# Performance work log

Measured on AMD Instinct MI355X. Metric: run time of the kernel, lower is better.

Reference implementation:

```python
import jax, jax.numpy as jnp
import numpy as np

ALPHA = 2.0
K_HOPS = 3
N_NODES, N_EDGES, IN_DIM = 8192, 131072, 128


def _mlp(coeffs, W0, W1, W2, W3):
    # MLP(n_layers=n_hidden_layers+2=4, relu between, no bias, bn/dropout off in eval)
    h = jax.nn.relu(coeffs @ W0)
    h = jax.nn.relu(h @ W1)
    h = jax.nn.relu(h @ W2)
    return h @ W3  # [N, 1] rotation angles


def _aggregate_k_hop(edge_index, angles):
    # Faithful translation of aggregate_k_hop including its in-place aliasing:
    # enhanced_angles aliases angles, and step_k ACCUMULATES across hops
    # (torch_scatter reduces into the provided out tensor).
    N = angles.shape[0]
    row, col = edge_index[0], edge_index[1]
    f = lambda k: jnp.exp(jnp.asarray(-ALPHA * k, angles.dtype))
    # hop 1: scatter-add over the raw edge list (duplicate edges counted, as in original)
    step = jax.ops.segment_sum(angles[col] * f(1), row, num_segments=N)
    enhanced = angles + step
    # Dense boolean adjacency: composing paths then np.unique(axis=1) is exactly the
    # 'exists a k-step walk' indicator, i.e. boolean adjacency powers.
    adj = jnp.zeros((N, N), jnp.float32).at[row, col].set(1.0)
    P = adj
    for k in range(2, K_HOPS + 1):
        P = ((P @ adj) > 0).astype(jnp.float32)  # unique k-walk pairs
        step = step + f(k) * (P @ enhanced)      # reads angles AFTER previous in-place add
        enhanced = enhanced + step               # step accumulates across hops
    return enhanced


def setup_inputs() -> dict:
    key = jax.random.key(0)
    k0, k1, k2, k3, k4, k5 = jax.random.split(key, 6)
    s = 1.0 / np.sqrt(IN_DIM)
    return {
        "coeffs": jax.random.normal(k0, (N_NODES, IN_DIM), jnp.float32),
        "W0": jax.random.normal(k1, (IN_DIM, IN_DIM), jnp.float32) * s,
        "W1": jax.random.normal(k2, (IN_DIM, IN_DIM), jnp.float32) * s,
        "W2": jax.random.normal(k3, (IN_DIM, IN_DIM), jnp.float32) * s,
        "W3": jax.random.normal(k4, (IN_DIM, 1), jnp.float32) * s,
        "edge_index": jax.random.randint(k5, (2, N_EDGES), 0, N_NODES, dtype=jnp.int32),
    }


def reference(coeffs, W0, W1, W2, W3, edge_index):
    angles = _mlp(coeffs, W0, W1, W2, W3)
    return _aggregate_k_hop(edge_index, angles)  # batch.node_rotation_angles, [N, 1]
```

## Files before the change

### kernel.cpp

```cpp
#include <hip/hip_runtime.h>

constexpr int N    = 8192;
constexpr int NE   = 131072;
constexpr int WPR  = N / 32;
constexpr int MAXD = 64;

#define F1 0.13533528323661270f
#define F2 0.018315638888734179f
#define F3 0.0024787521766663585f

using bf16x8 = __attribute__((ext_vector_type(8))) short;
using f32x4  = __attribute__((ext_vector_type(4))) float;

__device__ __forceinline__ unsigned short f2bf(float f) {
    unsigned int u = __float_as_uint(f);
    u = (u + 0x7FFFu + ((u >> 16) & 1u)) >> 16;
    return (unsigned short)u;
}

__global__ __launch_bounds__(256) void mlp_kernel(
    const float* __restrict__ X,
    const float* __restrict__ W0, const float* __restrict__ W1,
    const float* __restrict__ W2, const float* __restrict__ W3,
    float* __restrict__ angles, uint4* __restrict__ zbase)
{
    __shared__ unsigned short Xb[32 * 136];
    __shared__ unsigned short Wt[128 * 136];
    __shared__ float part[2][32];

    const int tid  = threadIdx.x;
    const int row0 = blockIdx.x * 32;
    const int w  = tid >> 6, l = tid & 63;
    const int mt = w & 1, nh = w >> 1;
    const int lm = l & 15, lq = l >> 4;

    if (tid < 16) {
        uint4 z; z.x = z.y = z.z = z.w = 0u;
        zbase[blockIdx.x * 16 + tid] = z;
    }

    for (int q = tid; q < 32 * 32; q += 256) {
        float4 v = *(const float4*)&X[row0 * 128 + q * 4];
        ushort4 b;
        b.x = f2bf(v.x); b.y = f2bf(v.y); b.z = f2bf(v.z); b.w = f2bf(v.w);
        *(ushort4*)&Xb[(q >> 5) * 136 + (q & 31) * 4] = b;
    }

    for (int layer = 0; layer < 3; ++layer) {
        const float* __restrict__ W = (layer == 0) ? W0 : (layer == 1) ? W1 : W2;
        for (int it = 0; it < 16; ++it) {
            int flat = it * 256 + tid;
            int n  = flat & 127;
            int k0 = (flat >> 7) << 2;
            ushort4 b;
            b.x = f2bf(W[(k0 + 0) * 128 + n]);
            b.y = f2bf(W[(k0 + 1) * 128 + n]);
            b.z = f2bf(W[(k0 + 2) * 128 + n]);
            b.w = f2bf(W[(k0 + 3) * 128 + n]);
            *(ushort4*)&Wt[n * 136 + k0] = b;
        }
        __syncthreads();

        f32x4 acc[4];
#pragma unroll
        for (int t = 0; t < 4; ++t) acc[t] = (f32x4){0.f, 0.f, 0.f, 0.f};

#pragma unroll
        for (int kc = 0; kc < 4; ++kc) {
            bf16x8 a = *(const bf16x8*)&Xb[(mt * 16 + lm) * 136 + kc * 32 + lq * 8];
#pragma unroll
            for (int t = 0; t < 4; ++t) {
                bf16x8 b = *(const bf16x8*)
                    &Wt[(nh * 64 + t * 16 + lm) * 136 + kc * 32 + lq * 8];
                acc[t] = __builtin_amdgcn_mfma_f32_16x16x32_bf16(a, b, acc[t], 0, 0, 0);
            }
        }

#pragma unroll
        for (int t = 0; t < 4; ++t)
#pragma unroll
            for (int r = 0; r < 4; ++r) acc[t][r] = fmaxf(acc[t][r], 0.0f);

        __syncthreads();

        if (layer < 2) {
#pragma unroll
            for (int t = 0; t < 4; ++t)
#pragma unroll
                for (int r = 0; r < 4; ++r)
                    Xb[(mt * 16 + lq * 4 + r) * 136 + nh * 64 + t * 16 + lm] =
                        f2bf(acc[t][r]);
        } else {
            float p[4] = {0.f, 0.f, 0.f, 0.f};
#pragma unroll
            for (int t = 0; t < 4; ++t) {
                float w3v = W3[nh * 64 + t * 16 + lm];
#pragma unroll
                for (int r = 0; r < 4; ++r) p[r] += acc[t][r] * w3v;
            }
#pragma unroll
            for (int r = 0; r < 4; ++r) {
                p[r] += __shfl_xor(p[r], 1, 64);
                p[r] += __shfl_xor(p[r], 2, 64);
                p[r] += __shfl_xor(p[r], 4, 64);
                p[r] += __shfl_xor(p[r], 8, 64);
            }
            if (lm == 0)
#pragma unroll
                for (int r = 0; r < 4; ++r)
                    part[nh][mt * 16 + lq * 4 + r] = p[r];
            __syncthreads();
            if (tid < 32) angles[row0 + tid] = part[0][tid] + part[1][tid];
        }
    }
}

__global__ void edges_kernel(const int* __restrict__ ei,
                             const float* __restrict__ angles,
                             float* __restrict__ s1,
                             int* __restrict__ cnt_g,
                             int* __restrict__ nbr_g)
{
    int e = blockIdx.x * blockDim.x + threadIdx.x;
    if (e < NE) {
        int r = ei[e];
        int c = ei[NE + e];
        int p = atomicAdd(&cnt_g[r], 1);
        if (p < MAXD) nbr_g[r * MAXD + p] = c;
        atomicAdd(&s1[r], F1 * angles[c]);
    }
}

__global__ __launch_bounds__(256) void p2_kernel(
    const int* __restrict__ cnt_g, const int* __restrict__ nbr_g,
    unsigned int* __restrict__ P2,
    const float* __restrict__ angles, const float* __restrict__ s1,
    float* __restrict__ s2, float* __restrict__ e2)
{
    __shared__ unsigned int bm[4][WPR];
    __shared__ int nbr[4][MAXD];
    __shared__ int nc[4][MAXD];

    const int wv  = threadIdx.x >> 6;
    const int l   = threadIdx.x & 63;
    const int i   = blockIdx.x * 4 + wv;
    const int qq  = l >> 4;
    const int sub = l & 15;

#pragma unroll
    for (int s = 0; s < 4; ++s) bm[wv][s * 64 + l] = 0u;

    const int n = min(cnt_g[i], MAXD);
    if (l < n) {
        int m = nbr_g[i * MAXD + l];
        nbr[wv][l] = m;
        nc[wv][l]  = min(cnt_g[m], MAXD);
    }
    __syncthreads();

    for (int q0 = 0; q0 < n; q0 += 4) {
        int q = q0 + qq;
        int m = 0, c2 = 0;
        if (q < n) { m = nbr[wv][q]; c2 = nc[wv][q]; }
        for (int s = sub; s < c2; s += 16) {
            int id = nbr_g[m * MAXD + s];
            atomicOr(&bm[wv][id >> 5], 1u << (id & 31));
        }
    }
    __syncthreads();

    unsigned int w[4];
#pragma unroll
    for (int s = 0; s < 4; ++s) {
        w[s] = bm[wv][s * 64 + l];
        P2[(size_t)i * WPR + s * 64 + l] = w[s];
    }

    float local = 0.0f;
#pragma unroll
    for (int s = 0; s < 4; ++s) {
        unsigned int ww = w[s];
        const int base = (s * 64 + l) * 32;
        while (ww) {
            int b = __ffs(ww) - 1;
            ww &= ww - 1;
            local += angles[base + b] + s1[base + b];
        }
    }
#pragma unroll
    for (int m = 1; m < 64; m <<= 1) local += __shfl_xor(local, m, 64);
    if (l == 0) {
        float e1i = angles[i] + s1[i];
        float s2v = s1[i] + F2 * local;
        s2[i] = s2v;
        e2[i] = e1i + s2v;
    }
}

__global__ __launch_bounds__(512) void p3_kernel(
    const unsigned int* __restrict__ P2,
    const int* __restrict__ cnt_g, const int* __restrict__ nbr_g,
    const float* __restrict__ e2, const float* __restrict__ s2,
    float* __restrict__ out)
{
    __shared__ float e2s[N];
    __shared__ int nbr[8][MAXD];

    const int tid = threadIdx.x;
    const int wv  = tid >> 6;
    const int l   = tid & 63;
    const int i   = blockIdx.x * 8 + wv;

    for (int q = tid; q < N / 4; q += 512)
        *(float4*)&e2s[q * 4] = *(const float4*)&e2[q * 4];

    const int n = min(cnt_g[i], MAXD);
    if (l < n) nbr[wv][l] = nbr_g[i * MAXD + l];
    __syncthreads();

    unsigned int w[4] = {0u, 0u, 0u, 0u};
    for (int q = 0; q < n; ++q) {
        const unsigned int* rowp = P2 + (size_t)nbr[wv][q] * WPR + l;
#pragma unroll
        for (int s = 0; s < 4; ++s) w[s] |= rowp[s * 64];
    }

    float local = 0.0f;
#pragma unroll
    for (int c = 0; c < 32; ++c) {
        unsigned int wd  = __shfl(w[c >> 3], ((c & 7) << 3) | (l >> 3), 64);
        unsigned int nib = wd >> ((l & 7) * 4);
        float4 v = *(const float4*)&e2s[c * 256 + l * 4];
        local += (nib & 1u) ? v.x : 0.0f;
        local += (nib & 2u) ? v.y : 0.0f;
        local += (nib & 4u) ? v.z : 0.0f;
        local += (nib & 8u) ? v.w : 0.0f;
    }
#pragma unroll
    for (int m = 1; m < 64; m <<= 1) local += __shfl_xor(local, m, 64);
    if (l == 0)
        out[i] = e2[i] + s2[i] + F3 * local;
}

extern "C" void kernel_launch(void* const* d_in, const int* in_sizes, int n_in,
                              void* d_out, int out_size, void* d_ws, size_t ws_size,
                              hipStream_t stream)
{
    const float* coeffs = (const float*)d_in[0];
    const float* W0     = (const float*)d_in[1];
    const float* W1     = (const float*)d_in[2];
    const float* W2     = (const float*)d_in[3];
    const float* W3     = (const float*)d_in[4];
    const int*   ei     = (const int*)  d_in[5];
    float* out = (float*)d_out;

    char* ws = (char*)d_ws;
    float*          angles = (float*)(ws + 0 * 32768);
    float*          s2     = (float*)(ws + 1 * 32768);
    float*          e2     = (float*)(ws + 2 * 32768);
    int*            nbr_g  = (int*)  (ws + (1u  << 20));
    float*          s1     = (float*)(ws + (4u  << 20));
    int*            cnt_g  = (int*)  (ws + (4u  << 20) + 32768);
    unsigned int*   P2     = (unsigned int*)(ws + (5u  << 20));

    mlp_kernel<<<N / 32, 256, 0, stream>>>(coeffs, W0, W1, W2, W3, angles,
                                           (uint4*)s1);

    edges_kernel<<<NE / 256, 256, 0, stream>>>(ei, angles, s1, cnt_g, nbr_g);
    p2_kernel<<<N / 4, 256, 0, stream>>>(cnt_g, nbr_g, P2, angles, s1, s2, e2);
    p3_kernel<<<N / 8, 512, 0, stream>>>(P2, cnt_g, nbr_g, e2, s2, out);
}
```

Before: 120.4 us.

## Halve MLP row tile, accumulate e1 directly, vectorize bitmap accesses

The MLP kernel now handles 16 rows per block with four waves splitting N, which doubles the grid to 512 blocks. Each block writes both angles and e1, and it zeroes cnt_g directly. Edge scatter now accumulates into e1 rather than s1, so p2 reads one array instead of two and precomputes e2+s2 as es. P2 rows are read and written as uint4, and p3 stages the OR-ed bitmap in shared memory rather than using shuffles. The aims are more parallelism in the MLP and fewer global loads, at the cost of more W-to-shared conversion work per row.

New measurement: 136.9 us. 1.14x slower.

```diff
diff --git a/kernel.cpp b/kernel.cpp
--- a/kernel.cpp
+++ b/kernel.cpp
@@ -22,24 +22,24 @@
     const float* __restrict__ X,
     const float* __restrict__ W0, const float* __restrict__ W1,
     const float* __restrict__ W2, const float* __restrict__ W3,
-    float* __restrict__ angles, uint4* __restrict__ zbase)
-{
-    __shared__ unsigned short Xb[32 * 136];
+    float* __restrict__ angles, float* __restrict__ e1,
+    uint4* __restrict__ cntz)
+{
+    __shared__ unsigned short Xb[16 * 136];
     __shared__ unsigned short Wt[128 * 136];
-    __shared__ float part[2][32];
+    __shared__ float part[4][16];
 
     const int tid  = threadIdx.x;
-    const int row0 = blockIdx.x * 32;
-    const int w  = tid >> 6, l = tid & 63;
-    const int mt = w & 1, nh = w >> 1;
+    const int row0 = blockIdx.x * 16;
+    const int nh = tid >> 6, l = tid & 63;
     const int lm = l & 15, lq = l >> 4;
 
-    if (tid < 16) {
+    if (tid < 4) {
         uint4 z; z.x = z.y = z.z = z.w = 0u;
-        zbase[blockIdx.x * 16 + tid] = z;
-    }
-
-    for (int q = tid; q < 32 * 32; q += 256) {
+        cntz[blockIdx.x * 4 + tid] = z;
+    }
+
+    for (int q = tid; q < 512; q += 256) {
         float4 v = *(const float4*)&X[row0 * 128 + q * 4];
         ushort4 b;
         b.x = f2bf(v.x); b.y = f2bf(v.y); b.z = f2bf(v.z); b.w = f2bf(v.w);
@@ -61,23 +61,23 @@
         }
         __syncthreads();
 
-        f32x4 acc[4];
-#pragma unroll
-        for (int t = 0; t < 4; ++t) acc[t] = (f32x4){0.f, 0.f, 0.f, 0.f};
+        f32x4 acc[2];
+#pragma unroll
+        for (int t = 0; t < 2; ++t) acc[t] = (f32x4){0.f, 0.f, 0.f, 0.f};
 
 #pragma unroll
         for (int kc = 0; kc < 4; ++kc) {
-            bf16x8 a = *(const bf16x8*)&Xb[(mt * 16 + lm) * 136 + kc * 32 + lq * 8];
-#pragma unroll
-            for (int t = 0; t < 4; ++t) {
+            bf16x8 a = *(const bf16x8*)&Xb[lm * 136 + kc * 32 + lq * 8];
+#pragma unroll
+            for (int t = 0; t < 2; ++t) {
                 bf16x8 b = *(const bf16x8*)
-                    &Wt[(nh * 64 + t * 16 + lm) * 136 + kc * 32 + lq * 8];
+                    &Wt[(nh * 32 + t * 16 + lm) * 136 + kc * 32 + lq * 8];
                 acc[t] = __builtin_amdgcn_mfma_f32_16x16x32_bf16(a, b, acc[t], 0, 0, 0);
             }
         }
 
 #pragma unroll
-        for (int t = 0; t < 4; ++t)
+        for (int t = 0; t < 2; ++t)
 #pragma unroll
             for (int r = 0; r < 4; ++r) acc[t][r] = fmaxf(acc[t][r], 0.0f);
 
@@ -85,16 +85,16 @@
 
         if (layer < 2) {
 #pragma unroll
-            for (int t = 0; t < 4; ++t)
+            for (int t = 0; t < 2; ++t)
 #pragma unroll
                 for (int r = 0; r < 4; ++r)
-                    Xb[(mt * 16 + lq * 4 + r) * 136 + nh * 64 + t * 16 + lm] =
+                    Xb[(lq * 4 + r) * 136 + nh * 32 + t * 16 + lm] =
                         f2bf(acc[t][r]);
         } else {
             float p[4] = {0.f, 0.f, 0.f, 0.f};
 #pragma unroll
-            for (int t = 0; t < 4; ++t) {
-                float w3v = W3[nh * 64 + t * 16 + lm];
+            for (int t = 0; t < 2; ++t) {
+                float w3v = W3[nh * 32 + t * 16 + lm];
 #pragma unroll
                 for (int r = 0; r < 4; ++r) p[r] += acc[t][r] * w3v;
             }
@@ -108,16 +108,20 @@
             if (lm == 0)
 #pragma unroll
                 for (int r = 0; r < 4; ++r)
-                    part[nh][mt * 16 + lq * 4 + r] = p[r];
+                    part[nh][lq * 4 + r] = p[r];
             __syncthreads();
-            if (tid < 32) angles[row0 + tid] = part[0][tid] + part[1][tid];
+            if (tid < 16) {
+                float v = part[0][tid] + part[1][tid] + part[2][tid] + part[3][tid];
+                angles[row0 + tid] = v;
+                e1[row0 + tid] = v;
+            }
         }
     }
 }
 
 __global__ void edges_kernel(const int* __restrict__ ei,
                              const float* __restrict__ angles,
-                             float* __restrict__ s1,
+                             float* __restrict__ e1,
                              int* __restrict__ cnt_g,
                              int* __restrict__ nbr_g)
 {
@@ -127,17 +131,17 @@
         int c = ei[NE + e];
         int p = atomicAdd(&cnt_g[r], 1);
         if (p < MAXD) nbr_g[r * MAXD + p] = c;
-        atomicAdd(&s1[r], F1 * angles[c]);
+        atomicAdd(&e1[r], F1 * angles[c]);
     }
 }
 
 __global__ __launch_bounds__(256) void p2_kernel(
     const int* __restrict__ cnt_g, const int* __restrict__ nbr_g,
     unsigned int* __restrict__ P2,
-    const float* __restrict__ angles, const float* __restrict__ s1,
-    float* __restrict__ s2, float* __restrict__ e2)
-{
-    __shared__ unsigned int bm[4][WPR];
+    const float* __restrict__ angles, const float* __restrict__ e1,
+    float* __restrict__ e2, float* __restrict__ es)
+{
+    __shared__ __align__(16) unsigned int bm[4][WPR];
     __shared__ int nbr[4][MAXD];
     __shared__ int nc[4][MAXD];
 
@@ -169,42 +173,41 @@
     }
     __syncthreads();
 
-    unsigned int w[4];
+    uint4 w4 = *(const uint4*)&bm[wv][4 * l];
+    *(uint4*)&P2[(size_t)i * WPR + 4 * l] = w4;
+
+    float local = 0.0f;
+    unsigned int wrd[4] = {w4.x, w4.y, w4.z, w4.w};
 #pragma unroll
     for (int s = 0; s < 4; ++s) {
-        w[s] = bm[wv][s * 64 + l];
-        P2[(size_t)i * WPR + s * 64 + l] = w[s];
-    }
-
-    float local = 0.0f;
-#pragma unroll
-    for (int s = 0; s < 4; ++s) {
-        unsigned int ww = w[s];
-        const int base = (s * 64 + l) * 32;
+        unsigned int ww = wrd[s];
+        const int base = (4 * l + s) * 32;
         while (ww) {
             int b = __ffs(ww) - 1;
             ww &= ww - 1;
-            local += angles[base + b] + s1[base + b];
+            local += e1[base + b];
         }
     }
 #pragma unroll
     for (int m = 1; m < 64; m <<= 1) local += __shfl_xor(local, m, 64);
     if (l == 0) {
-        float e1i = angles[i] + s1[i];
-        float s2v = s1[i] + F2 * local;
-        s2[i] = s2v;
+        float e1i = e1[i];
+        float s1i = e1i - angles[i];
+        float s2v = s1i + F2 * local;
         e2[i] = e1i + s2v;
+        es[i] = e1i + 2.0f * s2v;
     }
 }
 
 __global__ __launch_bounds__(512) void p3_kernel(
     const unsigned int* __restrict__ P2,
     const int* __restrict__ cnt_g, const int* __restrict__ nbr_g,
-    const float* __restrict__ e2, const float* __restrict__ s2,
+    const float* __restrict__ e2, const float* __restrict__ es,
     float* __restrict__ out)
 {
     __shared__ float e2s[N];
     __shared__ int nbr[8][MAXD];
+    __shared__ uint4 bmw[8][64];
 
     const int tid = threadIdx.x;
     const int wv  = tid >> 6;
@@ -218,17 +221,20 @@
     if (l < n) nbr[wv][l] = nbr_g[i * MAXD + l];
     __syncthreads();
 
-    unsigned int w[4] = {0u, 0u, 0u, 0u};
+    uint4 w; w.x = w.y = w.z = w.w = 0u;
     for (int q = 0; q < n; ++q) {
-        const unsigned int* rowp = P2 + (size_t)nbr[wv][q] * WPR + l;
-#pragma unroll
-        for (int s = 0; s < 4; ++s) w[s] |= rowp[s * 64];
-    }
-
+        const uint4* rowp = (const uint4*)(P2 + (size_t)nbr[wv][q] * WPR);
+        uint4 r = rowp[l];
+        w.x |= r.x; w.y |= r.y; w.z |= r.z; w.w |= r.w;
+    }
+    bmw[wv][l] = w;
+    __syncthreads();
+
+    const unsigned int* bw = (const unsigned int*)&bmw[wv][0];
     float local = 0.0f;
 #pragma unroll
     for (int c = 0; c < 32; ++c) {
-        unsigned int wd  = __shfl(w[c >> 3], ((c & 7) << 3) | (l >> 3), 64);
+        unsigned int wd  = bw[c * 8 + (l >> 3)];
         unsigned int nib = wd >> ((l & 7) * 4);
         float4 v = *(const float4*)&e2s[c * 256 + l * 4];
         local += (nib & 1u) ? v.x : 0.0f;
@@ -239,7 +245,7 @@
 #pragma unroll
     for (int m = 1; m < 64; m <<= 1) local += __shfl_xor(local, m, 64);
     if (l == 0)
-        out[i] = e2[i] + s2[i] + F3 * local;
+        out[i] = es[i] + F3 * local;
 }
 
 extern "C" void kernel_launch(void* const* d_in, const int* in_sizes, int n_in,
@@ -256,17 +262,17 @@
 
     char* ws = (char*)d_ws;
     float*          angles = (float*)(ws + 0 * 32768);
-    float*          s2     = (float*)(ws + 1 * 32768);
-    float*          e2     = (float*)(ws + 2 * 32768);
+    float*          e2     = (float*)(ws + 1 * 32768);
+    float*          es     = (float*)(ws + 2 * 32768);
     int*            nbr_g  = (int*)  (ws + (1u  << 20));
-    float*          s1     = (float*)(ws + (4u  << 20));
+    float*          e1     = (float*)(ws + (4u  << 20));
     int*            cnt_g  = (int*)  (ws + (4u  << 20) + 32768);
     unsigned int*   P2     = (unsigned int*)(ws + (5u  << 20));
 
-    mlp_kernel<<<N / 32, 256, 0, stream>>>(coeffs, W0, W1, W2, W3, angles,
-                                           (uint4*)s1);
-
-    edges_kernel<<<NE / 256, 256, 0, stream>>>(ei, angles, s1, cnt_g, nbr_g);
-    p2_kernel<<<N / 4, 256, 0, stream>>>(cnt_g, nbr_g, P2, angles, s1, s2, e2);
-    p3_kernel<<<N / 8, 512, 0, stream>>>(P2, cnt_g, nbr_g, e2, s2, out);
-}
+    mlp_kernel<<<N / 16, 256, 0, stream>>>(coeffs, W0, W1, W2, W3, angles, e1,
+                                           (uint4*)cnt_g);
+
+    edges_kernel<<<NE / 256, 256, 0, stream>>>(ei, angles, e1, cnt_g, nbr_g);
+    p2_kernel<<<N / 4, 256, 0, stream>>>(cnt_g, nbr_g, P2, angles, e1, e2, es);
+    p3_kernel<<<N / 8, 512, 0, stream>>>(P2, cnt_g, nbr_g, e2, es, out);
+}
```
